# Kernel tuning notes

Measured on AMD Instinct MI355X. Metric: run time of the kernel, lower is better.

Reference implementation:

```python
import jax, jax.numpy as jnp
import numpy as np


def setup_inputs() -> dict:
    key = jax.random.key(0)
    k1, k2, k3, k4 = jax.random.split(key, 4)
    d_in, d_out = 1024, 1024
    x = jax.random.normal(k1, (4, 2048, d_in), dtype=jnp.float32)
    # nn.Linear weights, stored as [d_in, d_out] for x @ W (torch stores transpose)
    s = 1.0 / np.sqrt(d_in)
    Wq = jax.random.normal(k2, (d_in, d_out), dtype=jnp.float32) * s
    Wk = jax.random.normal(k3, (d_in, d_out), dtype=jnp.float32) * s
    Wv = jax.random.normal(k4, (d_in, d_out), dtype=jnp.float32) * s
    return {"x": x, "Wq": Wq, "Wk": Wk, "Wv": Wv}


def reference(x, Wq, Wk, Wv):
    # x: [b, s, d_in]; projections (no bias)
    q = jnp.einsum('bsi,io->bso', x, Wq)
    k = jnp.einsum('bsi,io->bso', x, Wk)
    v = jnp.einsum('bsi,io->bso', x, Wv)
    d_out = k.shape[-1]
    scores = jnp.einsum('bqd,bkd->bqk', q, k) / jnp.sqrt(jnp.float32(d_out))
    seq_len = x.shape[1]
    causal = jnp.tril(jnp.ones((seq_len, seq_len), dtype=bool))  # [s, s]
    scores = jnp.where(causal[None, :, :], scores, -jnp.inf)
    weights = jax.nn.softmax(scores, axis=-1)
    return jnp.einsum('bqk,bkd->bqd', weights, v)
```

## Files before the change

### kernel.cpp

```cpp
#include <hip/hip_runtime.h>

typedef __attribute__((ext_vector_type(8))) short bf16x8;
typedef __attribute__((ext_vector_type(4))) float f32x4;
typedef unsigned int u32;

__device__ __forceinline__ unsigned short f2bf(float f) {
  union { float f; unsigned int u; } a; a.f = f;
  unsigned int u = a.u;
  u += 0x7FFFu + ((u >> 16) & 1u);
  return (unsigned short)(u >> 16);
}

__device__ __forceinline__ void gload16(const unsigned short* g, unsigned short* l) {
  __builtin_amdgcn_global_load_lds((const __attribute__((address_space(1))) u32*)g,
                                   (__attribute__((address_space(3))) u32*)l, 16, 0, 0);
}

#define BK 64

template<int MODE>
__global__ __launch_bounds__(256, 4)
void gemm_bt(const unsigned short* __restrict__ A,
             const unsigned short* __restrict__ Bm,
             float* __restrict__ Cf,
             float* __restrict__ Cf2,
             unsigned short* __restrict__ Cb,
             int K, long aBatch, long bBatch, long cBatch, float scale)
{
  constexpr int NI    = 2;
  constexpr int BROWS = 16;
  constexpr int BG    = 2;

  int z, bm0 = 0, bn, p = 0;
  if (MODE == 3) {
    int flat = blockIdx.x + 16 * blockIdx.y + 128 * blockIdx.z;
    int rm   = (flat & 7) * 64 + (flat >> 3);
    z  = rm >> 7;
    p  = (rm >> 4) & 7;
    bn = (rm & 15) * 64;
  } else {
    z   = blockIdx.z;
    bm0 = blockIdx.y * 128;
    bn  = blockIdx.x * 64;
  }

  A  += (long)z * aBatch;
  Bm += (long)z * bBatch;
  if (MODE == 3) { Cf += (long)z * cBatch; Cf2 += (long)z * 2048; }

  __shared__ __align__(16) unsigned short As[128 * BK];
  __shared__ __align__(16) unsigned short Bs[64 * BK];

  int tid  = threadIdx.x;
  int wave = tid >> 6, lane = tid & 63;
  int wm = wave * 32;
  int quad = lane >> 4, l16 = lane & 15;

  int r8 = lane >> 3;
  int c  = (lane & 7) ^ r8;
  const unsigned short* Bg = Bm + (long)(bn + wave * BROWS + r8) * K + c * 8;
  unsigned short* Al = &As[(wave * 32) * BK];
  unsigned short* Bl = &Bs[(wave * BROWS) * BK];

  const int nseg = (MODE == 3) ? 2 : 1;
  for (int seg = 0; seg < nseg; seg++) {
    int bm   = (MODE == 3) ? ((seg == 0) ? (15 - p) * 128 : p * 128) : bm0;
    int Keff = (MODE == 3) ? ((seg == 0) ? 128 * (16 - p) : 128 * (p + 1)) : K;
    const unsigned short* Ag = A + (long)(bm + wave * 32 + r8) * K + c * 8;

    f32x4 acc[NI][4] = {};

    for (int k0 = 0; k0 < Keff; k0 += BK) {
#pragma unroll
      for (int g = 0; g < 4; g++)
        gload16(Ag + k0 + (long)g * 8 * K, Al + g * 8 * BK);
#pragma unroll
      for (int g = 0; g < BG; g++)
        gload16(Bg + k0 + (long)g * 8 * K, Bl + g * 8 * BK);
      __syncthreads();

#pragma unroll
      for (int h = 0; h < 2; h++) {
        bf16x8 af[NI], bfr[4];
#pragma unroll
        for (int i = 0; i < NI; i++)
          af[i]  = *(const bf16x8*)&As[(wm + i * 16 + l16) * BK + (((quad + 4 * h) ^ (l16 & 7)) * 8)];
#pragma unroll
        for (int j = 0; j < 4; j++)
          bfr[j] = *(const bf16x8*)&Bs[(j * 16 + l16) * BK + (((quad + 4 * h) ^ (l16 & 7)) * 8)];
#pragma unroll
        for (int i = 0; i < NI; i++)
#pragma unroll
          for (int j = 0; j < 4; j++)
            acc[i][j] = __builtin_amdgcn_mfma_f32_16x16x32_bf16(af[i], bfr[j], acc[i][j], 0, 0, 0);
      }
      __syncthreads();
    }

#pragma unroll
    for (int i = 0; i < NI; i++) {
      int grow0 = bm + wm + i * 16 + quad * 4;
      if (MODE == 3) {
        float rinv[4];
#pragma unroll
        for (int r = 0; r < 4; r++) rinv[r] = 1.0f / Cf2[grow0 + r];
#pragma unroll
        for (int j = 0; j < 4; j++) {
          int gcol = bn + j * 16 + l16;
#pragma unroll
          for (int r = 0; r < 4; r++)
            Cf[(long)(grow0 + r) * 1024 + gcol] = acc[i][j][r] * rinv[r];
        }
      } else {
#pragma unroll
        for (int j = 0; j < 4; j++) {
          int gcol = bn + j * 16 + l16;
#pragma unroll
          for (int r = 0; r < 4; r++)
            Cb[(long)(grow0 + r) * 1024 + gcol] = f2bf(acc[i][j][r]);
        }
      }
    }
  }
}

__global__ __launch_bounds__(256, 4)
void mt64(const unsigned short* __restrict__ Wkb,
          const unsigned short* __restrict__ Wqb,
          unsigned short* __restrict__ Mt)
{
  int bm = blockIdx.y * 64, bn = blockIdx.x * 64;
  __shared__ __align__(16) unsigned short As[64 * 64];
  __shared__ __align__(16) unsigned short Bs[64 * 64];

  int tid  = threadIdx.x;
  int wave = tid >> 6, lane = tid & 63;
  int quad = lane >> 4, l16 = lane & 15;
  int r8 = lane >> 3;
  int c  = (lane & 7) ^ r8;
  const unsigned short* Ag = Wkb + (long)(bm + wave * 16 + r8) * 1024 + c * 8;
  const unsigned short* Bg = Wqb + (long)(bn + wave * 16 + r8) * 1024 + c * 8;
  unsigned short* Al = &As[(wave * 16) * 64];
  unsigned short* Bl = &Bs[(wave * 16) * 64];

  f32x4 acc[4] = {};

  for (int k0 = 0; k0 < 1024; k0 += 64) {
#pragma unroll
    for (int g = 0; g < 2; g++)
      gload16(Ag + k0 + (long)g * 8 * 1024, Al + g * 8 * 64);
#pragma unroll
    for (int g = 0; g < 2; g++)
      gload16(Bg + k0 + (long)g * 8 * 1024, Bl + g * 8 * 64);
    __syncthreads();

#pragma unroll
    for (int h = 0; h < 2; h++) {
      bf16x8 af, bfr[4];
      af = *(const bf16x8*)&As[(wave * 16 + l16) * 64 + (((quad + 4 * h) ^ (l16 & 7)) * 8)];
#pragma unroll
      for (int j = 0; j < 4; j++)
        bfr[j] = *(const bf16x8*)&Bs[(j * 16 + l16) * 64 + (((quad + 4 * h) ^ (l16 & 7)) * 8)];
#pragma unroll
      for (int j = 0; j < 4; j++)
        acc[j] = __builtin_amdgcn_mfma_f32_16x16x32_bf16(af, bfr[j], acc[j], 0, 0, 0);
    }
    __syncthreads();
  }

  int grow0 = bm + wave * 16 + quad * 4;
#pragma unroll
  for (int j = 0; j < 4; j++) {
    int gcol = bn + j * 16 + l16;
#pragma unroll
    for (int r = 0; r < 4; r++)
      Mt[(long)(grow0 + r) * 1024 + gcol] = f2bf(acc[j][r]);
  }
}

__global__ __launch_bounds__(128, 3)
void scores2wz(const unsigned short* __restrict__ T,
               const unsigned short* __restrict__ Xb,
               float* __restrict__ rsum,
               unsigned short* __restrict__ E,
               float scale)
{
  int flat = blockIdx.x + 272 * blockIdx.z;
  int rm   = (flat & 7) * 136 + (flat >> 3);
  int z = rm / 272;
  int f = rm % 272;
  int r = (int)((sqrtf((float)(4 * f + 1)) - 1.0f) * 0.5f);
  while ((r + 1) * (r + 2) <= f) r++;
  while (r * (r + 1) > f) r--;
  int bm0 = r * 128;
  int bn  = (f - r * (r + 1)) * 64;

  const unsigned short* A = T  + (long)z * 2048 * 1024;
  const unsigned short* B = Xb + (long)z * 2048 * 1024;
  unsigned short* Cb = E + (long)z * 2048 * 2048;
  float* Cf = rsum + (long)z * 2048;

  __shared__ __align__(16) unsigned short As[128 * BK];
  __shared__ __align__(16) unsigned short Bs[64 * BK];

  int tid  = threadIdx.x;
  int wave = tid >> 6, lane = tid & 63;
  int quad = lane >> 4, l16 = lane & 15;
  int wm   = wave * 64;

  int r8 = lane >> 3;
  int c  = (lane & 7) ^ r8;
  const unsigned short* Ag = A + (long)(bm0 + wave * 64 + r8) * 1024 + c * 8;
  const unsigned short* Bg = B + (long)(bn  + wave * 32 + r8) * 1024 + c * 8;
  unsigned short* Al = &As[(wave * 64) * BK];
  unsigned short* Bl = &Bs[(wave * 32) * BK];

  f32x4 acc[4][4] = {};

  for (int k0 = 0; k0 < 1024; k0 += BK) {
#pragma unroll
    for (int g = 0; g < 8; g++)
      gload16(Ag + k0 + (long)g * 8 * 1024, Al + g * 8 * BK);
#pragma unroll
    for (int g = 0; g < 4; g++)
      gload16(Bg + k0 + (long)g * 8 * 1024, Bl + g * 8 * BK);
    __syncthreads();

#pragma unroll
    for (int h = 0; h < 2; h++) {
      bf16x8 af[4], bfr[4];
#pragma unroll
      for (int i = 0; i < 4; i++)
        af[i]  = *(const bf16x8*)&As[(wm + i * 16 + l16) * BK + (((quad + 4 * h) ^ (l16 & 7)) * 8)];
#pragma unroll
      for (int j = 0; j < 4; j++)
        bfr[j] = *(const bf16x8*)&Bs[(j * 16 + l16) * BK + (((quad + 4 * h) ^ (l16 & 7)) * 8)];
#pragma unroll
      for (int i = 0; i < 4; i++)
#pragma unroll
        for (int j = 0; j < 4; j++)
          acc[i][j] = __builtin_amdgcn_mfma_f32_16x16x32_bf16(af[i], bfr[j], acc[i][j], 0, 0, 0);
    }
    __syncthreads();
  }

#pragma unroll
  for (int i = 0; i < 4; i++) {
    int grow0 = bm0 + wm + i * 16 + quad * 4;
#pragma unroll
    for (int rr = 0; rr < 4; rr++) {
      int grow = grow0 + rr;
      float rowpart = 0.f;
#pragma unroll
      for (int j = 0; j < 4; j++) {
        int gcol = bn + j * 16 + l16;
        float e = (gcol <= grow) ? __expf(acc[i][j][rr] * scale) : 0.f;
        rowpart += e;
        Cb[(long)grow * 2048 + gcol] = f2bf(e);
      }
      rowpart += __shfl_xor(rowpart, 1);
      rowpart += __shfl_xor(rowpart, 2);
      rowpart += __shfl_xor(rowpart, 4);
      rowpart += __shfl_xor(rowpart, 8);
      if (l16 == 0) atomicAdd(&Cf[grow], rowpart);
    }
  }
}

__global__ __launch_bounds__(256, 4)
void gemm_tv2(const unsigned short* __restrict__ A,
              const unsigned short* __restrict__ Bm,
              unsigned short* __restrict__ Cb)
{
  int bm0 = blockIdx.y * 128;
  int bn  = blockIdx.x * 128;

  __shared__ __align__(16) unsigned short As[128 * BK];
  __shared__ __align__(16) unsigned short Bs[128 * BK];

  int tid  = threadIdx.x;
  int wave = tid >> 6, lane = tid & 63;
  int wm = (wave >> 1) * 64;
  int wn = (wave & 1) * 64;
  int quad = lane >> 4, l16 = lane & 15;

  int r8 = lane >> 3;
  int c  = (lane & 7) ^ r8;
  const unsigned short* Ag = A  + (long)(bm0 + wave * 32 + r8) * 1024 + c * 8;
  const unsigned short* Bg = Bm + (long)(bn  + wave * 32 + r8) * 1024 + c * 8;
  unsigned short* Al = &As[(wave * 32) * BK];
  unsigned short* Bl = &Bs[(wave * 32) * BK];

  f32x4 acc[4][4] = {};

  for (int k0 = 0; k0 < 1024; k0 += BK) {
#pragma unroll
    for (int g = 0; g < 4; g++)
      gload16(Ag + k0 + (long)g * 8 * 1024, Al + g * 8 * BK);
#pragma unroll
    for (int g = 0; g < 4; g++)
      gload16(Bg + k0 + (long)g * 8 * 1024, Bl + g * 8 * BK);
    __syncthreads();

#pragma unroll
    for (int h = 0; h < 2; h++) {
      bf16x8 af[4], bfr[4];
#pragma unroll
      for (int i = 0; i < 4; i++)
        af[i]  = *(const bf16x8*)&As[(wm + i * 16 + l16) * BK + (((quad + 4 * h) ^ (l16 & 7)) * 8)];
#pragma unroll
      for (int j = 0; j < 4; j++)
        bfr[j] = *(const bf16x8*)&Bs[(wn + j * 16 + l16) * BK + (((quad + 4 * h) ^ (l16 & 7)) * 8)];
#pragma unroll
      for (int i = 0; i < 4; i++)
#pragma unroll
        for (int j = 0; j < 4; j++)
          acc[i][j] = __builtin_amdgcn_mfma_f32_16x16x32_bf16(af[i], bfr[j], acc[i][j], 0, 0, 0);
    }
    __syncthreads();
  }

#pragma unroll
  for (int i = 0; i < 4; i++) {
    int grow0 = bm0 + wm + i * 16 + quad * 4;
#pragma unroll
    for (int j = 0; j < 4; j++) {
      int gcol = bn + wn + j * 16 + l16;
      int which = gcol >> 10;
      int col = gcol & 1023;
      if (which == 0) {
#pragma unroll
        for (int r = 0; r < 4; r++)
          Cb[(long)(grow0 + r) * 1024 + col] = f2bf(acc[i][j][r]);
      } else {
        unsigned short* Vt = Cb + (long)8192 * 1024;
        int bb = grow0 >> 11, s = grow0 & 2047;
        ushort4 pk;
        pk.x = f2bf(acc[i][j][0]); pk.y = f2bf(acc[i][j][1]);
        pk.z = f2bf(acc[i][j][2]); pk.w = f2bf(acc[i][j][3]);
        *(ushort4*)(Vt + ((long)bb * 1024 + col) * 2048 + s) = pk;
      }
    }
  }
}

__global__ __launch_bounds__(256)
void prep(const float* __restrict__ x,
          const float* __restrict__ W0, const float* __restrict__ W1,
          const float* __restrict__ W2,
          unsigned short* __restrict__ Xb,
          unsigned short* __restrict__ Wqb, unsigned short* __restrict__ Wkb,
          unsigned short* __restrict__ WvT,
          float* __restrict__ rsum)
{
  __shared__ float tile[32][33];
  int b = blockIdx.x;
  if (b < 8192) {
    long i = ((long)b * 256 + threadIdx.x) * 4;
    float4 v = *(const float4*)(x + i);
    ushort4 o;
    o.x = f2bf(v.x); o.y = f2bf(v.y); o.z = f2bf(v.z); o.w = f2bf(v.w);
    *(ushort4*)(Xb + i) = o;
  } else if (b < 10240) {
    int t = b - 8192;
    const float* W    = (t < 1024) ? W0 : W1;
    unsigned short* D = (t < 1024) ? Wqb : Wkb;
    long i = ((long)(t & 1023) * 256 + threadIdx.x) * 4;
    float4 v = *(const float4*)(W + i);
    ushort4 o;
    o.x = f2bf(v.x); o.y = f2bf(v.y); o.z = f2bf(v.z); o.w = f2bf(v.w);
    *(ushort4*)(D + i) = o;
  } else if (b < 11264) {
    int q = b - 10240;
    int kb = (q >> 5) * 32, nb = (q & 31) * 32;
    int tx = threadIdx.x & 31, ty = threadIdx.x >> 5;
    for (int r = ty; r < 32; r += 8)
      tile[r][tx] = W2[(long)(kb + r) * 1024 + nb + tx];
    __syncthreads();
    for (int r = ty; r < 32; r += 8)
      WvT[(long)(nb + r) * 1024 + kb + tx] = f2bf(tile[tx][r]);
  } else {
    long i = ((long)(b - 11264) * 256 + threadIdx.x) * 4;
    float4 zz = {0.f, 0.f, 0.f, 0.f};
    *(float4*)(rsum + i) = zz;
  }
}

extern "C" void kernel_launch(void* const* d_in, const int* in_sizes, int n_in,
                              void* d_out, int out_size, void* d_ws, size_t ws_size,
                              hipStream_t stream) {
  const float* x  = (const float*)d_in[0];
  const float* Wq = (const float*)d_in[1];
  const float* Wk = (const float*)d_in[2];
  const float* Wv = (const float*)d_in[3];
  float* out = (float*)d_out;

  unsigned short* Xb  = (unsigned short*)d_ws;
  unsigned short* Wqb = Xb  + (long)8192 * 1024;
  unsigned short* Wkb = Wqb + (long)1024 * 1024;
  unsigned short* TVB = Wkb + (long)1024 * 1024;
  unsigned short* T   = TVB + (long)2048 * 1024;
  unsigned short* Vt  = T   + (long)8192 * 1024;
  unsigned short* E   = Vt  + (long)8192 * 1024;
  float* rsum         = (float*)(E + (long)4 * 2048 * 2048);

  prep<<<11272, 256, 0, stream>>>(x, Wq, Wk, Wv, Xb, Wqb, Wkb,
                                  TVB + (long)1024 * 1024, rsum);

  mt64<<<dim3(16, 16, 1), 256, 0, stream>>>(Wkb, Wqb, TVB);

  gemm_tv2<<<dim3(16, 64, 1), 256, 0, stream>>>(Xb, TVB, T);

  scores2wz<<<dim3(272, 1, 4), 128, 0, stream>>>(T, Xb, rsum, E, 0.03125f);

  gemm_bt<3><<<dim3(16, 8, 4), 256, 0, stream>>>(E, Vt, out, rsum, nullptr, 2048,
      (long)2048 * 2048, (long)1024 * 2048, (long)2048 * 1024, 1.f);
}
```

Measured before the change: 203.3 us.

## Replace paired-segment PV GEMM with 2-wave 64x64 per-wave tiles

```diff
diff --git a/kernel.cpp b/kernel.cpp
--- a/kernel.cpp
+++ b/kernel.cpp
@@ -17,112 +17,6 @@
 }
 
 #define BK 64
-
-template<int MODE>
-__global__ __launch_bounds__(256, 4)
-void gemm_bt(const unsigned short* __restrict__ A,
-             const unsigned short* __restrict__ Bm,
-             float* __restrict__ Cf,
-             float* __restrict__ Cf2,
-             unsigned short* __restrict__ Cb,
-             int K, long aBatch, long bBatch, long cBatch, float scale)
-{
-  constexpr int NI    = 2;
-  constexpr int BROWS = 16;
-  constexpr int BG    = 2;
-
-  int z, bm0 = 0, bn, p = 0;
-  if (MODE == 3) {
-    int flat = blockIdx.x + 16 * blockIdx.y + 128 * blockIdx.z;
-    int rm   = (flat & 7) * 64 + (flat >> 3);
-    z  = rm >> 7;
-    p  = (rm >> 4) & 7;
-    bn = (rm & 15) * 64;
-  } else {
-    z   = blockIdx.z;
-    bm0 = blockIdx.y * 128;
-    bn  = blockIdx.x * 64;
-  }
-
-  A  += (long)z * aBatch;
-  Bm += (long)z * bBatch;
-  if (MODE == 3) { Cf += (long)z * cBatch; Cf2 += (long)z * 2048; }
-
-  __shared__ __align__(16) unsigned short As[128 * BK];
-  __shared__ __align__(16) unsigned short Bs[64 * BK];
-
-  int tid  = threadIdx.x;
-  int wave = tid >> 6, lane = tid & 63;
-  int wm = wave * 32;
-  int quad = lane >> 4, l16 = lane & 15;
-
-  int r8 = lane >> 3;
-  int c  = (lane & 7) ^ r8;
-  const unsigned short* Bg = Bm + (long)(bn + wave * BROWS + r8) * K + c * 8;
-  unsigned short* Al = &As[(wave * 32) * BK];
-  unsigned short* Bl = &Bs[(wave * BROWS) * BK];
-
-  const int nseg = (MODE == 3) ? 2 : 1;
-  for (int seg = 0; seg < nseg; seg++) {
-    int bm   = (MODE == 3) ? ((seg == 0) ? (15 - p) * 128 : p * 128) : bm0;
-    int Keff = (MODE == 3) ? ((seg == 0) ? 128 * (16 - p) : 128 * (p + 1)) : K;
-    const unsigned short* Ag = A + (long)(bm + wave * 32 + r8) * K + c * 8;
-
-    f32x4 acc[NI][4] = {};
-
-    for (int k0 = 0; k0 < Keff; k0 += BK) {
-#pragma unroll
-      for (int g = 0; g < 4; g++)
-        gload16(Ag + k0 + (long)g * 8 * K, Al + g * 8 * BK);
-#pragma unroll
-      for (int g = 0; g < BG; g++)
-        gload16(Bg + k0 + (long)g * 8 * K, Bl + g * 8 * BK);
-      __syncthreads();
-
-#pragma unroll
-      for (int h = 0; h < 2; h++) {
-        bf16x8 af[NI], bfr[4];
-#pragma unroll
-        for (int i = 0; i < NI; i++)
-          af[i]  = *(const bf16x8*)&As[(wm + i * 16 + l16) * BK + (((quad + 4 * h) ^ (l16 & 7)) * 8)];
-#pragma unroll
-        for (int j = 0; j < 4; j++)
-          bfr[j] = *(const bf16x8*)&Bs[(j * 16 + l16) * BK + (((quad + 4 * h) ^ (l16 & 7)) * 8)];
-#pragma unroll
-        for (int i = 0; i < NI; i++)
-#pragma unroll
-          for (int j = 0; j < 4; j++)
-            acc[i][j] = __builtin_amdgcn_mfma_f32_16x16x32_bf16(af[i], bfr[j], acc[i][j], 0, 0, 0);
-      }
-      __syncthreads();
-    }
-
-#pragma unroll
-    for (int i = 0; i < NI; i++) {
-      int grow0 = bm + wm + i * 16 + quad * 4;
-      if (MODE == 3) {
-        float rinv[4];
-#pragma unroll
-        for (int r = 0; r < 4; r++) rinv[r] = 1.0f / Cf2[grow0 + r];
-#pragma unroll
-        for (int j = 0; j < 4; j++) {
-          int gcol = bn + j * 16 + l16;
-#pragma unroll
-          for (int r = 0; r < 4; r++)
-            Cf[(long)(grow0 + r) * 1024 + gcol] = acc[i][j][r] * rinv[r];
-        }
-      } else {
-#pragma unroll
-        for (int j = 0; j < 4; j++) {
-          int gcol = bn + j * 16 + l16;
-#pragma unroll
-          for (int r = 0; r < 4; r++)
-            Cb[(long)(grow0 + r) * 1024 + gcol] = f2bf(acc[i][j][r]);
-        }
-      }
-    }
-  }
-}
 
 __global__ __launch_bounds__(256, 4)
 void mt64(const unsigned short* __restrict__ Wkb,
@@ -340,6 +234,88 @@
         pk.z = f2bf(acc[i][j][2]); pk.w = f2bf(acc[i][j][3]);
         *(ushort4*)(Vt + ((long)bb * 1024 + col) * 2048 + s) = pk;
       }
+    }
+  }
+}
+
+__global__ __launch_bounds__(128, 3)
+void pv2w(const unsigned short* __restrict__ Em,
+          const unsigned short* __restrict__ Vt,
+          float* __restrict__ outp,
+          const float* __restrict__ rsum)
+{
+  int flat = blockIdx.x + 16 * blockIdx.y + 256 * blockIdx.z;
+  int rm   = (flat & 7) * 128 + (flat >> 3);
+  int z    = rm >> 8;
+  int w    = rm & 255;
+  int col  = w >> 4;
+  int q    = w & 15;
+  int s    = (q & 1) ? (q >> 1) : (15 - (q >> 1));
+  int bm   = s * 128;
+  int bn   = col * 64;
+  int Keff = (s + 1) * 128;
+
+  const unsigned short* A = Em + (long)z * 2048 * 2048;
+  const unsigned short* B = Vt + (long)z * 1024 * 2048;
+  float* C       = outp + (long)z * 2048 * 1024;
+  const float* R = rsum + (long)z * 2048;
+
+  __shared__ __align__(16) unsigned short As[128 * BK];
+  __shared__ __align__(16) unsigned short Bs[64 * BK];
+
+  int tid  = threadIdx.x;
+  int wave = tid >> 6, lane = tid & 63;
+  int quad = lane >> 4, l16 = lane & 15;
+  int wm   = wave * 64;
+
+  int r8 = lane >> 3;
+  int c  = (lane & 7) ^ r8;
+  const unsigned short* Ag = A + (long)(bm + wave * 64 + r8) * 2048 + c * 8;
+  const unsigned short* Bg = B + (long)(bn + wave * 32 + r8) * 2048 + c * 8;
+  unsigned short* Al = &As[(wave * 64) * BK];
+  unsigned short* Bl = &Bs[(wave * 32) * BK];
+
+  f32x4 acc[4][4] = {};
+
+  for (int k0 = 0; k0 < Keff; k0 += BK) {
+#pragma unroll
+    for (int g = 0; g < 8; g++)
+      gload16(Ag + k0 + (long)g * 8 * 2048, Al + g * 8 * BK);
+#pragma unroll
+    for (int g = 0; g < 4; g++)
+      gload16(Bg + k0 + (long)g * 8 * 2048, Bl + g * 8 * BK);
+    __syncthreads();
+
+#pragma unroll
+    for (int h = 0; h < 2; h++) {
+      bf16x8 af[4], bfr[4];
+#pragma unroll
+      for (int i = 0; i < 4; i++)
+        af[i]  = *(const bf16x8*)&As[(wm + i * 16 + l16) * BK + (((quad + 4 * h) ^ (l16 & 7)) * 8)];
+#pragma unroll
+      for (int j = 0; j < 4; j++)
+        bfr[j] = *(const bf16x8*)&Bs[(j * 16 + l16) * BK + (((quad + 4 * h) ^ (l16 & 7)) * 8)];
+#pragma unroll
+      for (int i = 0; i < 4; i++)
+#pragma unroll
+        for (int j = 0; j < 4; j++)
+          acc[i][j] = __builtin_amdgcn_mfma_f32_16x16x32_bf16(af[i], bfr[j], acc[i][j], 0, 0, 0);
+    }
+    __syncthreads();
+  }
+
+#pragma unroll
+  for (int i = 0; i < 4; i++) {
+    int grow0 = bm + wm + i * 16 + quad * 4;
+    float rinv[4];
+#pragma unroll
+    for (int r = 0; r < 4; r++) rinv[r] = 1.0f / R[grow0 + r];
+#pragma unroll
+    for (int j = 0; j < 4; j++) {
+      int gcol = bn + j * 16 + l16;
+#pragma unroll
+      for (int r = 0; r < 4; r++)
+        C[(long)(grow0 + r) * 1024 + gcol] = acc[i][j][r] * rinv[r];
     }
   }
 }
@@ -413,6 +389,5 @@
 
   scores2wz<<<dim3(272, 1, 4), 128, 0, stream>>>(T, Xb, rsum, E, 0.03125f);
 
-  gemm_bt<3><<<dim3(16, 8, 4), 256, 0, stream>>>(E, Vt, out, rsum, nullptr, 2048,
-      (long)2048 * 2048, (long)1024 * 2048, (long)2048 * 1024, 1.f);
-}
+  pv2w<<<dim3(16, 16, 4), 128, 0, stream>>>(E, Vt, out, rsum);
+}
```

After: 220.3 us. 1.08x slower.
